# Kernel tuning notes

Measured on AMD Instinct MI355X. Metric: run time of the kernel, lower is better.

Reference implementation:

```python
import jax, jax.numpy as jnp
import numpy as np
from jax import lax

MAX_DISP = 4  # patch_size = 2*MAX_DISP+1 = 9; kernel_size=1, stride=1, padding=0


def setup_inputs() -> dict:
    key = jax.random.key(0)
    k1, k2 = jax.random.split(key)
    B, C, H, W = 4, 256, 96, 96
    feat1 = jax.random.normal(k1, (B, C, H, W), dtype=jnp.float32)
    feat2 = jax.random.normal(k2, (B, C, H, W), dtype=jnp.float32)
    return {"feat1": feat1, "feat2": feat2}


def _cost_volume(feat1, feat2):
    # SpatialCorrelationSampler with kernel_size=1, patch_size=2*MAX_DISP+1,
    # stride=1, padding=0: for each displacement (dy,dx) in [-d,d]^2,
    # corr[b,dy,dx,y,x] = sum_c feat1[b,c,y,x] * feat2[b,c,y+dy,x+dx]
    # (out-of-bounds feat2 treated as zero). Output reshaped to [B, P*P, H, W].
    B, C, H, W = feat1.shape
    d = MAX_DISP
    P = 2 * d + 1
    f2_pad = jnp.pad(feat2, ((0, 0), (0, 0), (d, d), (d, d)))
    # flattened displacement offsets into the padded map, shape [P*P, 2]
    dy, dx = jnp.meshgrid(jnp.arange(P), jnp.arange(P), indexing="ij")
    offsets = jnp.stack([dy.ravel(), dx.ravel()], axis=-1)  # [P*P, 2]

    def step(carry, off):
        f2 = lax.dynamic_slice(f2_pad, (0, 0, off[0], off[1]), (B, C, H, W))
        corr = jnp.einsum("bchw,bchw->bhw", feat1, f2)  # sum over channels
        return carry, corr

    _, cv = lax.scan(step, None, offsets)  # [P*P, B, H, W]
    return jnp.transpose(cv, (1, 0, 2, 3))  # [B, P*P, H, W]


def reference(feat1, feat2):
    return _cost_volume(feat1, feat2)
```

## Files before the change

kernel.cpp:

```cpp
#include <hip/hip_runtime.h>


typedef _Float16 f16x8 __attribute__((ext_vector_type(8)));
typedef float f32x4 __attribute__((ext_vector_type(4)));

#define NB 4
#define NC 256
#define NH 96
#define NW 96
#define NP 9
#define PLANE (NH * NW)
#define TENS (NB * NH * NW * NC)
#define WS_NEED ((unsigned long long)TENS * 2ull)
#define TPT4 (TENS / 32)
#define PACK_BLK (TPT4 / 256)
#define MAIN_BLK 2304
#define CGSTR (NW * 8)
#define ROWSTR (32 * CGSTR)
#define AROW 272
#define LPAD 37

__global__ __launch_bounds__(256) void pack_f2(const float* __restrict__ f2,
                                               _Float16* __restrict__ ws)
{
    const int e   = blockIdx.x * 256 + threadIdx.x;
    const int row = e / 768;
    const int q   = e % 768;
    const int cg  = q / 24;
    const int x4  = q % 24;
    const int b   = row / NH;
    const int y   = row % NH;

    const float* sp = f2 + ((size_t)(b * NC + cg * 8) * NH + y) * NW + x4 * 4;
    float vv[8][4];
#pragma unroll
    for (int j = 0; j < 8; ++j) {
        const float4 v = *(const float4*)(sp + (size_t)j * PLANE);
        vv[j][0] = v.x; vv[j][1] = v.y; vv[j][2] = v.z; vv[j][3] = v.w;
    }
    _Float16* dp = ws + ((size_t)row * 32 + cg) * CGSTR + (size_t)x4 * 32;
#pragma unroll
    for (int xi = 0; xi < 4; ++xi) {
        f16x8 o;
#pragma unroll
        for (int j = 0; j < 8; ++j) o[j] = (_Float16)vv[j][xi];
        *(f16x8*)(dp + xi * 8) = o;
    }
}

__global__ __launch_bounds__(192) void costvol_mfma(const float* __restrict__ f1,
                                                    const _Float16* __restrict__ f2p,
                                                    float* __restrict__ out)
{
    __shared__ char shbuf[16 * AROW * 2];
    _Float16* lds_a = (_Float16*)shbuf;
    float (*ldso)[20] = (float(*)[20])shbuf;

    const int bid = blockIdx.x;
    const int swz = (bid & 7) * (MAIN_BLK / 8) + (bid >> 3);
    const int mt  = swz % 6;
    const int y   = (swz / 6) % 96;
    const int b   = swz / 576;

    const int w    = threadIdx.x >> 6;
    const int lane = threadIdx.x & 63;
    const int lr   = lane & 15;
    const int lg   = lane >> 4;
    const int m0   = mt * 16;

#pragma unroll
    for (int i = 0; i < 6; ++i) {
        const int task = threadIdx.x + i * 192;
        if (task < 1024) {
            const int c  = task >> 2;
            const int xq = task & 3;
            const float4 v = *(const float4*)(
                f1 + ((size_t)(b * NC + c) * NH + y) * NW + m0 + xq * 4);
            _Float16* d0 = lds_a + (size_t)(xq * 4) * AROW + c;
            d0[0 * AROW] = (_Float16)v.x;
            d0[1 * AROW] = (_Float16)v.y;
            d0[2 * AROW] = (_Float16)v.z;
            d0[3 * AROW] = (_Float16)v.w;
        }
    }
    __syncthreads();

    f16x8 a[8];
    {
        const _Float16* ap = lds_a + (size_t)lr * AROW + lg * 8;
#pragma unroll
        for (int ks = 0; ks < 8; ++ks) a[ks] = *(const f16x8*)(ap + ks * 32);
    }
    __syncthreads();

    const int n0a = m0 - 8 + lr;
    const int n0b = m0 + 8 + lr;
    const bool inA = (n0a >= 0);
    const bool inB = (n0b < 96);
    const f16x8 bz = {};

#pragma unroll 1
    for (int i = 0; i < 3; ++i) {
        const int dy = w * 3 + i;
        const int y2 = y + dy - 4;
        f32x4 acc0 = {0.f, 0.f, 0.f, 0.f};
        f32x4 acc1 = {0.f, 0.f, 0.f, 0.f};

        if (y2 >= 0 && y2 < 96) {
            const _Float16* base = f2p + (size_t)(b * 96 + y2) * ROWSTR + (size_t)lg * CGSTR;
            const _Float16* pba  = base + (ptrdiff_t)n0a * 8;
            const _Float16* pbb  = base + (ptrdiff_t)n0b * 8;
            f16x8 B0[8], B1[8];
#pragma unroll
            for (int ks = 0; ks < 8; ++ks) {
                B0[ks] = inA ? *(const f16x8*)(pba + (size_t)ks * 4 * CGSTR) : bz;
                B1[ks] = inB ? *(const f16x8*)(pbb + (size_t)ks * 4 * CGSTR) : bz;
            }
#pragma unroll
            for (int ks = 0; ks < 8; ++ks) {
                acc0 = __builtin_amdgcn_mfma_f32_16x16x32_f16(a[ks], B0[ks], acc0, 0, 0, 0);
                acc1 = __builtin_amdgcn_mfma_f32_16x16x32_f16(a[ks], B1[ks], acc1, 0, 0, 0);
            }
        }

#pragma unroll
        for (int reg = 0; reg < 4; ++reg) {
            const int mrow = lg * 4 + reg;
            const int dx0  = lr - mrow - 4;
            const int dx1  = dx0 + 16;
            if (dx0 >= 0 && dx0 <= 8) ldso[dy * 9 + dx0][mrow] = acc0[reg];
            if (dx1 >= 0 && dx1 <= 8) ldso[dy * 9 + dx1][mrow] = acc1[reg];
        }
    }

    __syncthreads();

    const int q = (threadIdx.x & 3) * 4;
#pragma unroll
    for (int r = threadIdx.x >> 2; r < 81; r += 48) {
        const float4 v = make_float4(ldso[r][q], ldso[r][q + 1],
                                     ldso[r][q + 2], ldso[r][q + 3]);
        *(float4*)(out + ((size_t)(b * 81 + r) * PLANE) + y * 96 + m0 + q) = v;
    }
}

__global__ __launch_bounds__(256) void costvol_f32(const float* __restrict__ f1,
                                                   const float* __restrict__ f2,
                                                   float* __restrict__ out)
{
    __shared__ float lds[2 * 64 * LPAD];
    const int bid = blockIdx.x;
    const int swz = (bid & 7) * (1296 / 8) + (bid >> 3);
    const int dyi = swz % NP;
    const int g   = swz / NP;
    const int w    = threadIdx.x >> 6;
    const int lane = threadIdx.x & 63;
    const int chk = g * 64 + lane;
    const int b   = chk / (NH * 24);
    const int rem = chk - b * (NH * 24);
    const int y   = rem / 24;
    const int x0  = (rem - y * 24) * 4;
    const int y2  = y + dyi - 4;

    float acc[NP][4];
#pragma unroll
    for (int i = 0; i < NP; ++i)
#pragma unroll
        for (int j = 0; j < 4; ++j) acc[i][j] = 0.f;

    if (y2 >= 0 && y2 < NH) {
        const float* p1 = f1 + ((size_t)(b * NC + w * 64) * NH + y) * NW + x0;
        const float* p2 = f2 + ((size_t)(b * NC + w * 64) * NH + y2) * NW + x0;
        const bool hasL = (x0 >= 4);
        const bool hasR = (x0 <= NW - 8);
#pragma unroll 4
        for (int c = 0; c < 64; ++c) {
            const float4 av = *(const float4*)p1;
            const float4 Lv = hasL ? *(const float4*)(p2 - 4) : make_float4(0.f, 0.f, 0.f, 0.f);
            const float4 Mv = *(const float4*)(p2);
            const float4 Rv = hasR ? *(const float4*)(p2 + 4) : make_float4(0.f, 0.f, 0.f, 0.f);
            const float wv[12] = {Lv.x, Lv.y, Lv.z, Lv.w, Mv.x, Mv.y, Mv.z, Mv.w,
                                  Rv.x, Rv.y, Rv.z, Rv.w};
            const float aa[4] = {av.x, av.y, av.z, av.w};
#pragma unroll
            for (int dxi = 0; dxi < NP; ++dxi)
#pragma unroll
                for (int j = 0; j < 4; ++j) acc[dxi][j] += aa[j] * wv[dxi + j];
            p1 += PLANE;
            p2 += PLANE;
        }
    }

    float* reg0 = &lds[0 * 64 * LPAD + lane * LPAD];
    float* reg1 = &lds[1 * 64 * LPAD + lane * LPAD];
    if (w >= 2) {
        float* dst = (w == 2) ? reg0 : reg1;
#pragma unroll
        for (int dxi = 0; dxi < NP; ++dxi)
#pragma unroll
            for (int j = 0; j < 4; ++j) dst[dxi * 4 + j] = acc[dxi][j];
    }
    __syncthreads();
    if (w < 2) {
        const float* src = (w == 0) ? reg0 : reg1;
#pragma unroll
        for (int dxi = 0; dxi < NP; ++dxi)
#pragma unroll
            for (int j = 0; j < 4; ++j) acc[dxi][j] += src[dxi * 4 + j];
    }
    __syncthreads();
    if (w == 1) {
#pragma unroll
        for (int dxi = 0; dxi < NP; ++dxi)
#pragma unroll
            for (int j = 0; j < 4; ++j) reg0[dxi * 4 + j] = acc[dxi][j];
    }
    __syncthreads();
    if (w == 0) {
#pragma unroll
        for (int dxi = 0; dxi < NP; ++dxi)
#pragma unroll
            for (int j = 0; j < 4; ++j) acc[dxi][j] += reg0[dxi * 4 + j];
        float* ob = out + ((size_t)(b * 81 + dyi * 9) * NH + y) * NW + x0;
#pragma unroll
        for (int dxi = 0; dxi < NP; ++dxi) {
            *(float4*)ob = make_float4(acc[dxi][0], acc[dxi][1], acc[dxi][2], acc[dxi][3]);
            ob += PLANE;
        }
    }
}

extern "C" void kernel_launch(void* const* d_in, const int* in_sizes, int n_in,
                              void* d_out, int out_size, void* d_ws, size_t ws_size,
                              hipStream_t stream) {
    const float* f1 = (const float*)d_in[0];
    const float* f2 = (const float*)d_in[1];
    float* out = (float*)d_out;
    if (ws_size >= WS_NEED) {
        _Float16* ws = (_Float16*)d_ws;
        pack_f2<<<dim3(PACK_BLK, 1, 1), dim3(256, 1, 1), 0, stream>>>(f2, ws);
        costvol_mfma<<<dim3(MAIN_BLK, 1, 1), dim3(192, 1, 1), 0, stream>>>(f1, ws, out);
    } else {
        costvol_f32<<<dim3(1296, 1, 1), dim3(256, 1, 1), 0, stream>>>(f1, f2, out);
    }
}
```

Baseline: 38.52 us.

## Software-pipeline f2 loads across dy rows with double-buffered register halves

Replaces the serial per-dy loop in the MFMA kernel with a fully unrolled software pipeline. B-operand loads for the next dy (split into two K-halves P/Q) are issued before the MFMAs of the current half, so global latency overlaps compute. It also moves the f2 loads ahead of the A-fragment LDS reads. The A tile and the output staging buffer now use separate shared arrays, which drops the second __syncthreads at the cost of more LDS per block and higher register pressure.

```diff
diff --git a/kernel.cpp b/kernel.cpp
--- a/kernel.cpp
+++ b/kernel.cpp
@@ -52,9 +52,8 @@
                                                     const _Float16* __restrict__ f2p,
                                                     float* __restrict__ out)
 {
-    __shared__ char shbuf[16 * AROW * 2];
-    _Float16* lds_a = (_Float16*)shbuf;
-    float (*ldso)[20] = (float(*)[20])shbuf;
+    __shared__ _Float16 lds_a[16 * AROW];
+    __shared__ float ldso[81][20];
 
     const int bid = blockIdx.x;
     const int swz = (bid & 7) * (MAIN_BLK / 8) + (bid >> 3);
@@ -85,53 +84,86 @@
     }
     __syncthreads();
 
-    f16x8 a[8];
-    {
-        const _Float16* ap = lds_a + (size_t)lr * AROW + lg * 8;
-#pragma unroll
-        for (int ks = 0; ks < 8; ++ks) a[ks] = *(const f16x8*)(ap + ks * 32);
-    }
-    __syncthreads();
-
     const int n0a = m0 - 8 + lr;
     const int n0b = m0 + 8 + lr;
     const bool inA = (n0a >= 0);
     const bool inB = (n0b < 96);
     const f16x8 bz = {};
 
-#pragma unroll 1
-    for (int i = 0; i < 3; ++i) {
-        const int dy = w * 3 + i;
-        const int y2 = y + dy - 4;
-        f32x4 acc0 = {0.f, 0.f, 0.f, 0.f};
-        f32x4 acc1 = {0.f, 0.f, 0.f, 0.f};
-
-        if (y2 >= 0 && y2 < 96) {
-            const _Float16* base = f2p + (size_t)(b * 96 + y2) * ROWSTR + (size_t)lg * CGSTR;
-            const _Float16* pba  = base + (ptrdiff_t)n0a * 8;
-            const _Float16* pbb  = base + (ptrdiff_t)n0b * 8;
-            f16x8 B0[8], B1[8];
-#pragma unroll
-            for (int ks = 0; ks < 8; ++ks) {
-                B0[ks] = inA ? *(const f16x8*)(pba + (size_t)ks * 4 * CGSTR) : bz;
-                B1[ks] = inB ? *(const f16x8*)(pbb + (size_t)ks * 4 * CGSTR) : bz;
-            }
-#pragma unroll
-            for (int ks = 0; ks < 8; ++ks) {
-                acc0 = __builtin_amdgcn_mfma_f32_16x16x32_f16(a[ks], B0[ks], acc0, 0, 0, 0);
-                acc1 = __builtin_amdgcn_mfma_f32_16x16x32_f16(a[ks], B1[ks], acc1, 0, 0, 0);
-            }
-        }
-
-#pragma unroll
-        for (int reg = 0; reg < 4; ++reg) {
-            const int mrow = lg * 4 + reg;
-            const int dx0  = lr - mrow - 4;
-            const int dx1  = dx0 + 16;
-            if (dx0 >= 0 && dx0 <= 8) ldso[dy * 9 + dx0][mrow] = acc0[reg];
-            if (dx1 >= 0 && dx1 <= 8) ldso[dy * 9 + dx1][mrow] = acc1[reg];
-        }
-    }
+    const _Float16* f2base = f2p + (size_t)(b * 96) * ROWSTR + (size_t)lg * CGSTR;
+    const int y20 = y + (w * 3 + 0) - 4;
+    const int y21 = y + (w * 3 + 1) - 4;
+    const int y22 = y + (w * 3 + 2) - 4;
+    const bool v0 = (y20 >= 0) && (y20 < 96);
+    const bool v1 = (y21 >= 0) && (y21 < 96);
+    const bool v2 = (y22 >= 0) && (y22 < 96);
+    const ptrdiff_t ro0 = (ptrdiff_t)(v0 ? y20 : 0) * ROWSTR;
+    const ptrdiff_t ro1 = (ptrdiff_t)(v1 ? y21 : 0) * ROWSTR;
+    const ptrdiff_t ro2 = (ptrdiff_t)(v2 ? y22 : 0) * ROWSTR;
+
+#define LOADH(BUF, V, RO, H)                                                   \
+    {                                                                          \
+        if (V) {                                                               \
+            const _Float16* _ba = f2base + (RO) + (ptrdiff_t)n0a * 8;          \
+            const _Float16* _bb = f2base + (RO) + (ptrdiff_t)n0b * 8;          \
+            _Pragma("unroll") for (int t = 0; t < 4; ++t) {                    \
+                BUF[t]     = inA ? *(const f16x8*)(_ba + ((H) * 4 + t) * 4 * CGSTR) : bz; \
+                BUF[t + 4] = inB ? *(const f16x8*)(_bb + ((H) * 4 + t) * 4 * CGSTR) : bz; \
+            }                                                                  \
+        } else {                                                               \
+            _Pragma("unroll") for (int t = 0; t < 8; ++t) BUF[t] = bz;         \
+        }                                                                      \
+    }
+
+#define MFMAH(BUF, H)                                                          \
+    {                                                                          \
+        _Pragma("unroll") for (int t = 0; t < 4; ++t) {                        \
+            acc0 = __builtin_amdgcn_mfma_f32_16x16x32_f16(a[(H) * 4 + t], BUF[t],     acc0, 0, 0, 0); \
+            acc1 = __builtin_amdgcn_mfma_f32_16x16x32_f16(a[(H) * 4 + t], BUF[t + 4], acc1, 0, 0, 0); \
+        }                                                                      \
+    }
+
+#define STAGE(D)                                                               \
+    {                                                                          \
+        const int dyv = w * 3 + (D);                                           \
+        _Pragma("unroll") for (int reg = 0; reg < 4; ++reg) {                  \
+            const int mrow = lg * 4 + reg;                                     \
+            const int dx0  = lr - mrow - 4;                                    \
+            const int dx1  = dx0 + 16;                                         \
+            if (dx0 >= 0 && dx0 <= 8) ldso[dyv * 9 + dx0][mrow] = acc0[reg];   \
+            if (dx1 >= 0 && dx1 <= 8) ldso[dyv * 9 + dx1][mrow] = acc1[reg];   \
+        }                                                                      \
+        acc0 = (f32x4){0.f, 0.f, 0.f, 0.f};                                   \
+        acc1 = (f32x4){0.f, 0.f, 0.f, 0.f};                                   \
+    }
+
+    f16x8 P[8], Q[8];
+    f32x4 acc0 = {0.f, 0.f, 0.f, 0.f};
+    f32x4 acc1 = {0.f, 0.f, 0.f, 0.f};
+
+    LOADH(P, v0, ro0, 0);
+    LOADH(Q, v0, ro0, 1);
+
+    f16x8 a[8];
+    {
+        const _Float16* ap = lds_a + (size_t)lr * AROW + lg * 8;
+#pragma unroll
+        for (int ks = 0; ks < 8; ++ks) a[ks] = *(const f16x8*)(ap + ks * 32);
+    }
+
+    MFMAH(P, 0);
+    LOADH(P, v1, ro1, 0);
+    MFMAH(Q, 1);
+    LOADH(Q, v1, ro1, 1);
+    STAGE(0);
+    MFMAH(P, 0);
+    LOADH(P, v2, ro2, 0);
+    MFMAH(Q, 1);
+    LOADH(Q, v2, ro2, 1);
+    STAGE(1);
+    MFMAH(P, 0);
+    MFMAH(Q, 1);
+    STAGE(2);
 
     __syncthreads();
 
@@ -142,6 +174,9 @@
                                      ldso[r][q + 2], ldso[r][q + 3]);
         *(float4*)(out + ((size_t)(b * 81 + r) * PLANE) + y * 96 + m0 + q) = v;
     }
+#undef LOADH
+#undef MFMAH
+#undef STAGE
 }
 
 __global__ __launch_bounds__(256) void costvol_f32(const float* __restrict__ f1,
```

New measurement: 40.61 us. +5.4%, slower.

## Split MFMA cost-volume work across six waves, one N-tile per wave

Applied to the files above, without the earlier changes.

Doubles the block to 384 threads so each wave handles one of the two 16-column feat2 tiles for its three dy rows, instead of one wave computing both tiles. The f1 staging buffer and the output staging buffer now live in separate LDS arrays, which removes the barrier that previously separated A-fragment reads from output writes. The intent is more waves in flight for latency hiding and fewer live B registers per wave. The cost is that each wave now loads its own copy of the A fragments, and the block uses more LDS. The change also adds an unused variable whose name contains a non-ASCII character.

```diff
diff --git a/kernel.cpp b/kernel.cpp
--- a/kernel.cpp
+++ b/kernel.cpp
@@ -48,13 +48,12 @@
     }
 }
 
-__global__ __launch_bounds__(192) void costvol_mfma(const float* __restrict__ f1,
+__global__ __launch_bounds__(384) void costvol_mfma(const float* __restrict__ f1,
                                                     const _Float16* __restrict__ f2p,
                                                     float* __restrict__ out)
 {
-    __shared__ char shbuf[16 * AROW * 2];
-    _Float16* lds_a = (_Float16*)shbuf;
-    float (*ldso)[20] = (float(*)[20])shbuf;
+    __shared__ _Float16 lds_a[16 * AROW];
+    __shared__ float ldso[81][20];
 
     const int bid = blockIdx.x;
     const int swz = (bid & 7) * (MAIN_BLK / 8) + (bid >> 3);
@@ -67,10 +66,12 @@
     const int lr   = lane & 15;
     const int lg   = lane >> 4;
     const int m0   = mt * 16;
-
-#pragma unroll
-    for (int i = 0; i < 6; ++i) {
-        const int task = threadIdx.x + i * 192;
+    const int d3   = w >> 1;
+    const int tl   = w & 1;
+
+#pragma unroll
+    for (int i = 0; i < 3; ++i) {
+        const int task = threadIdx.x + i * 384;
         if (task < 1024) {
             const int c  = task >> 2;
             const int xq = task & 3;
@@ -91,53 +92,43 @@
 #pragma unroll
         for (int ks = 0; ks < 8; ++ks) a[ks] = *(const f16x8*)(ap + ks * 32);
     }
-    __syncthreads();
-
-    const int n0a = m0 - 8 + lr;
-    const int n0b = m0 + 8 + lr;
-    const bool inA = (n0a >= 0);
-    const bool inB = (n0b < 96);
+
+    const int n0   = m0 + (tl ? 8 : -8) + lr;
+    const bool inN = tl ? (n0 < 96) : (n0 >= 0);
+    const int dxoف = 0;
     const f16x8 bz = {};
 
 #pragma unroll 1
     for (int i = 0; i < 3; ++i) {
-        const int dy = w * 3 + i;
+        const int dy = d3 * 3 + i;
         const int y2 = y + dy - 4;
-        f32x4 acc0 = {0.f, 0.f, 0.f, 0.f};
-        f32x4 acc1 = {0.f, 0.f, 0.f, 0.f};
+        f32x4 acc = {0.f, 0.f, 0.f, 0.f};
 
         if (y2 >= 0 && y2 < 96) {
-            const _Float16* base = f2p + (size_t)(b * 96 + y2) * ROWSTR + (size_t)lg * CGSTR;
-            const _Float16* pba  = base + (ptrdiff_t)n0a * 8;
-            const _Float16* pbb  = base + (ptrdiff_t)n0b * 8;
-            f16x8 B0[8], B1[8];
-#pragma unroll
-            for (int ks = 0; ks < 8; ++ks) {
-                B0[ks] = inA ? *(const f16x8*)(pba + (size_t)ks * 4 * CGSTR) : bz;
-                B1[ks] = inB ? *(const f16x8*)(pbb + (size_t)ks * 4 * CGSTR) : bz;
-            }
-#pragma unroll
-            for (int ks = 0; ks < 8; ++ks) {
-                acc0 = __builtin_amdgcn_mfma_f32_16x16x32_f16(a[ks], B0[ks], acc0, 0, 0, 0);
-                acc1 = __builtin_amdgcn_mfma_f32_16x16x32_f16(a[ks], B1[ks], acc1, 0, 0, 0);
-            }
+            const _Float16* pb = f2p + (size_t)(b * 96 + y2) * ROWSTR
+                               + (size_t)lg * CGSTR + (ptrdiff_t)n0 * 8;
+            f16x8 B[8];
+#pragma unroll
+            for (int ks = 0; ks < 8; ++ks)
+                B[ks] = inN ? *(const f16x8*)(pb + (size_t)ks * 4 * CGSTR) : bz;
+#pragma unroll
+            for (int ks = 0; ks < 8; ++ks)
+                acc = __builtin_amdgcn_mfma_f32_16x16x32_f16(a[ks], B[ks], acc, 0, 0, 0);
         }
 
 #pragma unroll
         for (int reg = 0; reg < 4; ++reg) {
             const int mrow = lg * 4 + reg;
-            const int dx0  = lr - mrow - 4;
-            const int dx1  = dx0 + 16;
-            if (dx0 >= 0 && dx0 <= 8) ldso[dy * 9 + dx0][mrow] = acc0[reg];
-            if (dx1 >= 0 && dx1 <= 8) ldso[dy * 9 + dx1][mrow] = acc1[reg];
-        }
-    }
-
-    __syncthreads();
-
+            const int dx   = lr - mrow + (tl ? 12 : -4);
+            if (dx >= 0 && dx <= 8) ldso[dy * 9 + dx][mrow] = acc[reg];
+        }
+    }
+
+    __syncthreads();
+
+    const int r = threadIdx.x >> 2;
     const int q = (threadIdx.x & 3) * 4;
-#pragma unroll
-    for (int r = threadIdx.x >> 2; r < 81; r += 48) {
+    if (r < 81) {
         const float4 v = make_float4(ldso[r][q], ldso[r][q + 1],
                                      ldso[r][q + 2], ldso[r][q + 3]);
         *(float4*)(out + ((size_t)(b * 81 + r) * PLANE) + y * 96 + m0 + q) = v;
@@ -239,7 +230,7 @@
     if (ws_size >= WS_NEED) {
         _Float16* ws = (_Float16*)d_ws;
         pack_f2<<<dim3(PACK_BLK, 1, 1), dim3(256, 1, 1), 0, stream>>>(f2, ws);
-        costvol_mfma<<<dim3(MAIN_BLK, 1, 1), dim3(192, 1, 1), 0, stream>>>(f1, ws, out);
+        costvol_mfma<<<dim3(MAIN_BLK, 1, 1), dim3(384, 1, 1), 0, stream>>>(f1, ws, out);
     } else {
         costvol_f32<<<dim3(1296, 1, 1), dim3(256, 1, 1), 0, stream>>>(f1, f2, out);
     }
```

Measured after the change: 38.95 us. Within noise of the previous version (+1.1%).
